# Kernel tuning notes

Hardware: AMD Instinct MI355X
Metric: run time of the kernel (lower is better)

## Reference

```python
import jax, jax.numpy as jnp
import numpy as np

WS = 7          # window size
SHIFT = 3       # shift size (window_size // 2)
RES = 56        # input resolution
DIMS = 192      # channel dim
HEADS = DIMS // 32
HD = DIMS // HEADS
N = WS * WS     # tokens per window (49)
NW = (RES // WS) ** 2  # windows per image (64)


def _position_index():
    # matches tf.meshgrid(coords_w, coords_h)[::-1] stacking
    coords = np.stack(np.meshgrid(np.arange(WS), np.arange(WS))[::-1])  # (2, ws, ws)
    flat = coords.reshape(2, -1)                                        # (2, N)
    rel = (flat[:, :, None] - flat[:, None, :]).transpose(1, 2, 0)      # (N, N, 2)
    h = (rel[..., 0] + WS - 1) * (2 * WS - 1)
    w = rel[..., 1] + WS - 1
    return (h + w).reshape(-1)                                          # (N*N,)


def _swin_mask():
    img = np.zeros((RES, RES))
    cnt = 0
    sls = (slice(0, -WS), slice(-WS, -SHIFT), slice(-SHIFT, None))
    for hs in sls:
        for ws_ in sls:
            img[hs, ws_] = cnt
            cnt += 1
    # window partition
    m = img.reshape(RES // WS, WS, RES // WS, WS).transpose(0, 2, 1, 3).reshape(-1, N)
    a = m[:, None, :] - m[:, :, None]            # (nW, N, N)
    a = np.where(a == 0, 0.0, -1000.0).astype(np.float32)
    return a[:, None]                            # (nW, 1, N, N)


_PIDX = _position_index()
_MASK = _swin_mask()


def setup_inputs() -> dict:
    key = jax.random.key(0)
    ks = jax.random.split(key, 6)
    s = 0.02
    return {
        "x": jax.random.normal(ks[0], (64, RES, RES, DIMS), jnp.float32),
        "table": jax.random.normal(ks[1], ((2 * WS - 1) ** 2, HEADS), jnp.float32) * s,
        "wq": jax.random.normal(ks[2], (DIMS, DIMS), jnp.float32) * s,
        "bq": jnp.zeros((DIMS,), jnp.float32),
        "wk": jax.random.normal(ks[3], (DIMS, DIMS), jnp.float32) * s,
        "bk": jnp.zeros((DIMS,), jnp.float32),
        "wv": jax.random.normal(ks[4], (DIMS, DIMS), jnp.float32) * s,
        "bv": jnp.zeros((DIMS,), jnp.float32),
        "wo": jax.random.normal(ks[5], (DIMS, DIMS), jnp.float32) * s,
        "bo": jnp.zeros((DIMS,), jnp.float32),
    }


def reference(x, table, wq, bq, wk, bk, wv, bv, wo, bo):
    B = x.shape[0]
    # gathered relative-position bias: (1, heads, N, N)
    bias = table[_PIDX].reshape(N, N, HEADS).transpose(2, 0, 1)[None]
    mask = jnp.asarray(_MASK)  # (nW, 1, N, N)

    # cyclic shift + window partition
    xs = jnp.roll(x, (-SHIFT, -SHIFT), axis=(1, 2))
    xw = xs.reshape(B, RES // WS, WS, RES // WS, WS, DIMS)
    xw = xw.transpose(0, 1, 3, 2, 4, 5).reshape(-1, N, DIMS)  # (B*nW, N, C)
    BW = xw.shape[0]

    def split_heads(t):
        return t.reshape(BW, N, HEADS, HD).transpose(0, 2, 1, 3)  # (BW, h, N, hd)

    q = split_heads(xw @ wq + bq)
    k = split_heads(xw @ wk + bk)
    v = split_heads(xw @ wv + bv)

    scores = jnp.einsum('bhqd,bhkd->bhqk', q, k) / jnp.sqrt(jnp.float32(HD))
    scores = scores + bias
    # matches tf.repeat(mask, B // W, axis=0) in the original code
    scores = scores + jnp.repeat(mask, BW // NW, axis=0)
    attn = jax.nn.softmax(scores, axis=-1)
    o = jnp.einsum('bhqk,bhkd->bhqd', attn, v)
    o = o.transpose(0, 2, 1, 3).reshape(BW, N, DIMS)
    o = o @ wo + bo

    # window reverse + reverse cyclic shift
    o = o.reshape(B, RES // WS, RES // WS, WS, WS, DIMS)
    o = o.transpose(0, 1, 3, 2, 4, 5).reshape(B, RES, RES, DIMS)
    return jnp.roll(o, (SHIFT, SHIFT), axis=(1, 2))
```

## Files before the change

### kernel.cpp

```cpp
#include <hip/hip_runtime.h>


typedef __attribute__((ext_vector_type(8))) short bf16x8;
typedef __attribute__((ext_vector_type(4))) short short4v;
typedef __attribute__((ext_vector_type(4))) float f32x4;

__device__ __forceinline__ short f2bf(float x) {
  unsigned u = __builtin_bit_cast(unsigned, x);
  u += 0x7fffu + ((u >> 16) & 1u);
  return (short)(u >> 16);
}

__global__ void prep_kernel(const float* __restrict__ wq, const float* __restrict__ wk,
                            const float* __restrict__ wv, const float* __restrict__ wo,
                            const float* __restrict__ table,
                            short* __restrict__ wT, float* __restrict__ biasx) {
  int tid = blockIdx.x * 256 + threadIdx.x;
  if (tid < 4 * 36864) {
    int mat = tid / 36864, rem = tid % 36864;
    int k = rem / 192, n = rem % 192;
    const float* w = (mat == 0) ? wq : (mat == 1) ? wk : (mat == 2) ? wv : wo;
    wT[mat * 36864 + n * 192 + k] = f2bf(w[k * 192 + n]);
  }
  if (tid < 6 * 2401) {
    int h = tid / 2401, rem = tid % 2401;
    int q = rem / 49, k = rem % 49;
    int idx = ((q / 7) - (k / 7) + 6) * 13 + ((q % 7) - (k % 7) + 6);
    biasx[tid] = table[idx * 6 + h];
  }
}

__launch_bounds__(768, 3)
__global__ void swin_attn_kernel(const float* __restrict__ x,
                                 const short* __restrict__ wT,
                                 const float* __restrict__ biasx,
                                 const float* __restrict__ bq, const float* __restrict__ bk,
                                 const float* __restrict__ bv, const float* __restrict__ bo,
                                 float* __restrict__ out) {
  extern __shared__ short smem[];
  short* s_xw = smem;
  short* s_q  = smem + 12800;
  short* s_k  = smem + 25600;
  short* s_vt = smem + 38400;
  short* s_p  = smem + 52224;

  const int tid  = threadIdx.x;
  const int w    = tid >> 6;
  const int lane = tid & 63;
  const int quad = lane >> 4;
  const int l15  = lane & 15;

  const int bw  = blockIdx.x;
  const int b   = bw >> 6;
  const int wi  = bw & 63;
  const int wwh = wi >> 3, www = wi & 7;
  const int mwh = b >> 3,  mww = b & 7;

  for (int i = tid; i < 49 * 48; i += 768) {
    int t = i / 48, c4 = i - t * 48;
    int th = t / 7, tw = t - th * 7;
    int gh = wwh * 7 + th + 3; if (gh >= 56) gh -= 56;
    int gw = www * 7 + tw + 3; if (gw >= 56) gw -= 56;
    const float4 v = *(const float4*)(x + (((b * 56 + gh) * 56 + gw) * 192 + c4 * 4));
    short4v s;
    ((short*)&s)[0] = f2bf(v.x); ((short*)&s)[1] = f2bf(v.y);
    ((short*)&s)[2] = f2bf(v.z); ((short*)&s)[3] = f2bf(v.w);
    *(short4v*)(s_xw + t * 200 + c4 * 4) = s;
  }
  __syncthreads();

  const f32x4 zero4 = {0.f, 0.f, 0.f, 0.f};

  {
    const int mat = w >> 2;
    const short* wt = wT + mat * 36864;
    const float* bias = (mat == 0) ? bq : (mat == 1) ? bk : bv;

    bf16x8 axw[4][6];
#pragma unroll
    for (int mt = 0; mt < 4; ++mt)
#pragma unroll
      for (int ks = 0; ks < 6; ++ks)
        axw[mt][ks] = *(const bf16x8*)(s_xw + (mt * 16 + l15) * 200 + ks * 32 + quad * 8);

#pragma unroll
    for (int i = 0; i < 3; ++i) {
      const int col = ((w & 3) * 3 + i) * 16 + l15;
      f32x4 acc[4] = {zero4, zero4, zero4, zero4};
#pragma unroll
      for (int ks = 0; ks < 6; ++ks) {
        bf16x8 bfr = *(const bf16x8*)(wt + col * 192 + ks * 32 + quad * 8);
#pragma unroll
        for (int mt = 0; mt < 4; ++mt)
          acc[mt] = __builtin_amdgcn_mfma_f32_16x16x32_bf16(axw[mt][ks], bfr, acc[mt], 0, 0, 0);
      }
      const float bv_ = bias[col];
      if (mat < 2) {
        short* dst = (mat == 0) ? s_q : s_k;
#pragma unroll
        for (int mt = 0; mt < 4; ++mt)
#pragma unroll
          for (int r = 0; r < 4; ++r)
            dst[(mt * 16 + quad * 4 + r) * 200 + col] = f2bf(acc[mt][r] + bv_);
      } else {
#pragma unroll
        for (int mt = 0; mt < 4; ++mt) {
          short4v vv;
#pragma unroll
          for (int r = 0; r < 4; ++r) {
            int m = mt * 16 + quad * 4 + r;
            float val = (m < 49) ? (acc[mt][r] + bv_) : 0.f;
            ((short*)&vv)[r] = f2bf(val);
          }
          *(short4v*)(s_vt + col * 72 + mt * 16 + quad * 4) = vv;
        }
      }
    }
  }
  __syncthreads();

  const int rt = w & 3;
  const int hp = w >> 2;

  int cm[4], mclamp[4];
#pragma unroll
  for (int r = 0; r < 4; ++r) {
    int m = rt * 16 + quad * 4 + r;
    int mm = (m < 49) ? m : 48;
    mclamp[r] = mm * 49;
    int th = mm / 7, tw = mm - th * 7;
    int ch = (mwh == 7) ? (1 + (th >= 4)) : 0;
    int cw = (mww == 7) ? (1 + (tw >= 4)) : 0;
    cm[r] = ch * 3 + cw;
  }
  int cn[4], nclamp[4], nvalid[4];
#pragma unroll
  for (int nt = 0; nt < 4; ++nt) {
    int n = nt * 16 + l15;
    nvalid[nt] = (n < 49);
    int nn = nvalid[nt] ? n : 48;
    nclamp[nt] = nn;
    int th = nn / 7, tw = nn - th * 7;
    int ch = (mwh == 7) ? (1 + (th >= 4)) : 0;
    int cw = (mww == 7) ? (1 + (tw >= 4)) : 0;
    cn[nt] = ch * 3 + cw;
  }

  short* my_p = s_p + w * (16 * 72);
  const float SCALE = 0.17677669529663687f;
  const float NEGINF = -__builtin_inff();

#pragma unroll
  for (int hh = 0; hh < 2; ++hh) {
    const int h = hp * 2 + hh;
    const int d0 = h * 32;
    bf16x8 qf = *(const bf16x8*)(s_q + (rt * 16 + l15) * 200 + d0 + quad * 8);
    float sv[4][4];
#pragma unroll
    for (int nt = 0; nt < 4; ++nt) {
      bf16x8 kf = *(const bf16x8*)(s_k + (nt * 16 + l15) * 200 + d0 + quad * 8);
      f32x4 sfr = __builtin_amdgcn_mfma_f32_16x16x32_bf16(qf, kf, zero4, 0, 0, 0);
#pragma unroll
      for (int r = 0; r < 4; ++r) {
        float v = sfr[r] * SCALE + biasx[h * 2401 + mclamp[r] + nclamp[nt]]
                + ((cm[r] == cn[nt]) ? 0.f : -1000.f);
        sv[nt][r] = nvalid[nt] ? v : NEGINF;
      }
    }
    float inv[4];
#pragma unroll
    for (int r = 0; r < 4; ++r) {
      float mx = fmaxf(fmaxf(sv[0][r], sv[1][r]), fmaxf(sv[2][r], sv[3][r]));
#pragma unroll
      for (int d = 1; d < 16; d <<= 1) mx = fmaxf(mx, __shfl_xor(mx, d));
      float s0 = 0.f;
#pragma unroll
      for (int nt = 0; nt < 4; ++nt) {
        float e = __expf(sv[nt][r] - mx);
        sv[nt][r] = e;
        s0 += e;
      }
#pragma unroll
      for (int d = 1; d < 16; d <<= 1) s0 += __shfl_xor(s0, d);
      inv[r] = 1.0f / s0;
    }
#pragma unroll
    for (int nt = 0; nt < 4; ++nt)
#pragma unroll
      for (int r = 0; r < 4; ++r)
        my_p[(quad * 4 + r) * 72 + nt * 16 + l15] = f2bf(sv[nt][r]);

    f32x4 of[2] = {zero4, zero4};
#pragma unroll
    for (int ks = 0; ks < 2; ++ks) {
      bf16x8 pf = *(const bf16x8*)(my_p + l15 * 72 + ks * 32 + quad * 8);
#pragma unroll
      for (int nt2 = 0; nt2 < 2; ++nt2) {
        bf16x8 vf = *(const bf16x8*)(s_vt + (d0 + nt2 * 16 + l15) * 72 + ks * 32 + quad * 8);
        of[nt2] = __builtin_amdgcn_mfma_f32_16x16x32_bf16(pf, vf, of[nt2], 0, 0, 0);
      }
    }
#pragma unroll
    for (int nt2 = 0; nt2 < 2; ++nt2)
#pragma unroll
      for (int r = 0; r < 4; ++r)
        s_xw[(rt * 16 + quad * 4 + r) * 200 + d0 + nt2 * 16 + l15] = f2bf(of[nt2][r] * inv[r]);
  }
  __syncthreads();

  const int cg = hp;

  bf16x8 ao[6];
#pragma unroll
  for (int ks = 0; ks < 6; ++ks)
    ao[ks] = *(const bf16x8*)(s_xw + (rt * 16 + l15) * 200 + ks * 32 + quad * 8);

  int rowbase[4], rvalid[4];
#pragma unroll
  for (int r = 0; r < 4; ++r) {
    int m = rt * 16 + quad * 4 + r;
    rvalid[r] = (m < 49);
    int mm = rvalid[r] ? m : 0;
    int th = mm / 7, tw = mm - th * 7;
    int gh = wwh * 7 + th + 3; if (gh >= 56) gh -= 56;
    int gw = www * 7 + tw + 3; if (gw >= 56) gw -= 56;
    rowbase[r] = ((b * 56 + gh) * 56 + gw) * 192;
  }

  const short* wto = wT + 3 * 36864;
#pragma unroll
  for (int i = 0; i < 4; ++i) {
    const int col = (cg * 4 + i) * 16 + l15;
    f32x4 acc = zero4;
#pragma unroll
    for (int ks = 0; ks < 6; ++ks) {
      bf16x8 bfr = *(const bf16x8*)(wto + col * 192 + ks * 32 + quad * 8);
      acc = __builtin_amdgcn_mfma_f32_16x16x32_bf16(ao[ks], bfr, acc, 0, 0, 0);
    }
    const float bo_ = bo[col];
#pragma unroll
    for (int r = 0; r < 4; ++r)
      if (rvalid[r]) out[rowbase[r] + col] = acc[r] + bo_;
  }
}

extern "C" void kernel_launch(void* const* d_in, const int* in_sizes, int n_in,
                              void* d_out, int out_size, void* d_ws, size_t ws_size,
                              hipStream_t stream) {
  const float* x     = (const float*)d_in[0];
  const float* table = (const float*)d_in[1];
  const float* wq    = (const float*)d_in[2];
  const float* bq    = (const float*)d_in[3];
  const float* wk    = (const float*)d_in[4];
  const float* bk    = (const float*)d_in[5];
  const float* wv    = (const float*)d_in[6];
  const float* bv    = (const float*)d_in[7];
  const float* wo    = (const float*)d_in[8];
  const float* bo    = (const float*)d_in[9];
  float* out = (float*)d_out;

  short* wT    = (short*)d_ws;
  float* biasx = (float*)((char*)d_ws + 294912);

  prep_kernel<<<576, 256, 0, stream>>>(wq, wk, wv, wo, table, wT, biasx);

  const int smem_bytes = 66048 * 2;
  (void)hipFuncSetAttribute(reinterpret_cast<const void*>(swin_attn_kernel),
                            hipFuncAttributeMaxDynamicSharedMemorySize, smem_bytes);
  swin_attn_kernel<<<4096, 768, smem_bytes, stream>>>(x, wT, biasx, bq, bk, bv, bo, out);
}
```

Before: 589.0 us.

## Make attention kernel persistent over 16 windows with double-buffered input prefetch

Each block now processes 16 windows of one image in a loop instead of one window, launching 256 blocks instead of 4096. The next window's input is loaded into registers during attention and written to the alternate shared buffer, overlapping global loads with compute. Bias and mask terms are precomputed once per block in registers, and the QKV and output projections are remapped so each wave owns a token row tile with transposed MFMA operands, giving vectorized stores. The cost is only 256 blocks on a large GPU, roughly one block per CU, plus higher register pressure from the cached bias and prefetch registers.

```diff
diff --git a/kernel.cpp b/kernel.cpp
--- a/kernel.cpp
+++ b/kernel.cpp
@@ -38,11 +38,11 @@
                                  const float* __restrict__ bv, const float* __restrict__ bo,
                                  float* __restrict__ out) {
   extern __shared__ short smem[];
-  short* s_xw = smem;
-  short* s_q  = smem + 12800;
-  short* s_k  = smem + 25600;
-  short* s_vt = smem + 38400;
-  short* s_p  = smem + 52224;
+  short* bufA = smem;
+  short* bufB = smem + 13824;
+  short* s_q  = smem + 27648;
+  short* s_k  = smem + 40448;
+  short* s_vt = smem + 53248;
 
   const int tid  = threadIdx.x;
   const int w    = tid >> 6;
@@ -50,197 +50,269 @@
   const int quad = lane >> 4;
   const int l15  = lane & 15;
 
-  const int bw  = blockIdx.x;
-  const int b   = bw >> 6;
-  const int wi  = bw & 63;
-  const int wwh = wi >> 3, www = wi & 7;
-  const int mwh = b >> 3,  mww = b & 7;
-
-  for (int i = tid; i < 49 * 48; i += 768) {
+  const int p   = blockIdx.x;
+  const int b   = p >> 2;
+  const int mwh = b >> 3, mww = b & 7;
+
+  const int rt = w & 3;
+  const int g  = w >> 2;
+
+  const f32x4 zero4 = {0.f, 0.f, 0.f, 0.f};
+  const float NEGINF = -__builtin_inff();
+  const float SCALE = 0.17677669529663687f;
+
+  int th_[4], tw_[4], wa_[4], c4_[4];
+#pragma unroll
+  for (int it = 0; it < 4; ++it) {
+    int i = tid + it * 768;
     int t = i / 48, c4 = i - t * 48;
-    int th = t / 7, tw = t - th * 7;
-    int gh = wwh * 7 + th + 3; if (gh >= 56) gh -= 56;
-    int gw = www * 7 + tw + 3; if (gw >= 56) gw -= 56;
-    const float4 v = *(const float4*)(x + (((b * 56 + gh) * 56 + gw) * 192 + c4 * 4));
-    short4v s;
-    ((short*)&s)[0] = f2bf(v.x); ((short*)&s)[1] = f2bf(v.y);
-    ((short*)&s)[2] = f2bf(v.z); ((short*)&s)[3] = f2bf(v.w);
-    *(short4v*)(s_xw + t * 200 + c4 * 4) = s;
+    th_[it] = t / 7; tw_[it] = t - th_[it] * 7;
+    c4_[it] = c4; wa_[it] = t * 200 + c4 * 4;
+  }
+  const bool has4 = (tid < 48);
+
+  const int token = rt * 16 + l15;
+  const bool tokv = (token < 49);
+
+  const int qc  = tokv ? token : 48;
+  const int qth = qc / 7, qtw = qc - qth * 7;
+  const int cq  = ((mwh == 7) ? (1 + (qth >= 4)) : 0) * 3
+                + ((mww == 7) ? (1 + (qtw >= 4)) : 0);
+  float bm[2][4][4];
+#pragma unroll
+  for (int hh = 0; hh < 2; ++hh) {
+    const int h = g * 2 + hh;
+#pragma unroll
+    for (int mt = 0; mt < 4; ++mt)
+#pragma unroll
+      for (int r = 0; r < 4; ++r) {
+        int key = mt * 16 + quad * 4 + r;
+        if (key > 48) {
+          bm[hh][mt][r] = NEGINF;
+        } else {
+          int kth = key / 7, ktw = key - kth * 7;
+          int ck = ((mwh == 7) ? (1 + (kth >= 4)) : 0) * 3
+                 + ((mww == 7) ? (1 + (ktw >= 4)) : 0);
+          bm[hh][mt][r] = biasx[h * 2401 + qc * 49 + key] + ((ck == cq) ? 0.f : -1000.f);
+        }
+      }
+  }
+
+  const int tt  = tokv ? token : 0;
+  const int tth = tt / 7, ttw = tt - tth * 7;
+
+  {
+    const int wi0 = (p & 3) * 16;
+    const int hb = (wi0 >> 3) * 7 + 3, wb = (wi0 & 7) * 7 + 3;
+#pragma unroll
+    for (int it = 0; it < 3; ++it) {
+      int gh = hb + th_[it]; if (gh >= 56) gh -= 56;
+      int gw = wb + tw_[it]; if (gw >= 56) gw -= 56;
+      float4 v = *(const float4*)(x + (((b * 56 + gh) * 56 + gw) * 192 + c4_[it] * 4));
+      short4v s;
+      s[0] = f2bf(v.x); s[1] = f2bf(v.y); s[2] = f2bf(v.z); s[3] = f2bf(v.w);
+      *(short4v*)(bufA + wa_[it]) = s;
+    }
+    if (has4) {
+      int gh = hb + th_[3]; if (gh >= 56) gh -= 56;
+      int gw = wb + tw_[3]; if (gw >= 56) gw -= 56;
+      float4 v = *(const float4*)(x + (((b * 56 + gh) * 56 + gw) * 192 + c4_[3] * 4));
+      short4v s;
+      s[0] = f2bf(v.x); s[1] = f2bf(v.y); s[2] = f2bf(v.z); s[3] = f2bf(v.w);
+      *(short4v*)(bufA + wa_[3]) = s;
+    }
   }
   __syncthreads();
 
-  const f32x4 zero4 = {0.f, 0.f, 0.f, 0.f};
-
-  {
-    const int mat = w >> 2;
-    const short* wt = wT + mat * 36864;
-    const float* bias = (mat == 0) ? bq : (mat == 1) ? bk : bv;
-
-    bf16x8 axw[4][6];
-#pragma unroll
-    for (int mt = 0; mt < 4; ++mt)
-#pragma unroll
-      for (int ks = 0; ks < 6; ++ks)
-        axw[mt][ks] = *(const bf16x8*)(s_xw + (mt * 16 + l15) * 200 + ks * 32 + quad * 8);
-
-#pragma unroll
-    for (int i = 0; i < 3; ++i) {
-      const int col = ((w & 3) * 3 + i) * 16 + l15;
-      f32x4 acc[4] = {zero4, zero4, zero4, zero4};
+  float4 px0, px1, px2, px3;
+
+#pragma unroll 1
+  for (int win = 0; win < 16; ++win) {
+    short* xw   = (win & 1) ? bufB : bufA;
+    short* pbuf = (win & 1) ? bufA : bufB;
+    const int wi  = (p & 3) * 16 + win;
+    const int wwh = wi >> 3, www = wi & 7;
+
+    bf16x8 xf[6];
+#pragma unroll
+    for (int ks = 0; ks < 6; ++ks)
+      xf[ks] = *(const bf16x8*)(xw + (rt * 16 + l15) * 200 + ks * 32 + quad * 8);
+
+#pragma unroll
+    for (int mat = 0; mat < 2; ++mat) {
+      const short* wt = wT + mat * 36864;
+      const float* bp = mat ? bk : bq;
+      short* dst = mat ? s_k : s_q;
+#pragma unroll
+      for (int j = 0; j < 4; ++j) {
+        const int dbase = (g * 4 + j) * 16;
+        const short* wrow = wt + (dbase + l15) * 192;
+        f32x4 acc = zero4;
+#pragma unroll
+        for (int ks = 0; ks < 6; ++ks) {
+          bf16x8 wfr = *(const bf16x8*)(wrow + ks * 32 + quad * 8);
+          acc = __builtin_amdgcn_mfma_f32_16x16x32_bf16(wfr, xf[ks], acc, 0, 0, 0);
+        }
+        const float4 b4 = *(const float4*)(bp + dbase + quad * 4);
+        short4v st;
+        st[0] = f2bf(tokv ? acc[0] + b4.x : 0.f);
+        st[1] = f2bf(tokv ? acc[1] + b4.y : 0.f);
+        st[2] = f2bf(tokv ? acc[2] + b4.z : 0.f);
+        st[3] = f2bf(tokv ? acc[3] + b4.w : 0.f);
+        *(short4v*)(dst + (rt * 16 + l15) * 200 + dbase + quad * 4) = st;
+      }
+    }
+    {
+      const short* wt = wT + 2 * 36864;
+#pragma unroll
+      for (int j = 0; j < 4; ++j) {
+        const int dbase = (g * 4 + j) * 16;
+        const short* wrow = wt + (dbase + l15) * 192;
+        f32x4 acc = zero4;
+#pragma unroll
+        for (int ks = 0; ks < 6; ++ks) {
+          bf16x8 wfr = *(const bf16x8*)(wrow + ks * 32 + quad * 8);
+          acc = __builtin_amdgcn_mfma_f32_16x16x32_bf16(xf[ks], wfr, acc, 0, 0, 0);
+        }
+        const float bvv = bv[dbase + l15];
+        short4v st;
+#pragma unroll
+        for (int r = 0; r < 4; ++r) {
+          int key = rt * 16 + quad * 4 + r;
+          st[r] = f2bf((key < 49) ? (acc[r] + bvv) : 0.f);
+        }
+        *(short4v*)(s_vt + (dbase + l15) * 72 + rt * 16 + quad * 4) = st;
+      }
+    }
+    __syncthreads();
+
+    if (win < 15) {
+      const int wi2 = wi + 1;
+      const int hb = (wi2 >> 3) * 7 + 3, wb = (wi2 & 7) * 7 + 3;
+      {
+        int gh = hb + th_[0]; if (gh >= 56) gh -= 56;
+        int gw = wb + tw_[0]; if (gw >= 56) gw -= 56;
+        px0 = *(const float4*)(x + (((b * 56 + gh) * 56 + gw) * 192 + c4_[0] * 4));
+      }
+      {
+        int gh = hb + th_[1]; if (gh >= 56) gh -= 56;
+        int gw = wb + tw_[1]; if (gw >= 56) gw -= 56;
+        px1 = *(const float4*)(x + (((b * 56 + gh) * 56 + gw) * 192 + c4_[1] * 4));
+      }
+      {
+        int gh = hb + th_[2]; if (gh >= 56) gh -= 56;
+        int gw = wb + tw_[2]; if (gw >= 56) gw -= 56;
+        px2 = *(const float4*)(x + (((b * 56 + gh) * 56 + gw) * 192 + c4_[2] * 4));
+      }
+      if (has4) {
+        int gh = hb + th_[3]; if (gh >= 56) gh -= 56;
+        int gw = wb + tw_[3]; if (gw >= 56) gw -= 56;
+        px3 = *(const float4*)(x + (((b * 56 + gh) * 56 + gw) * 192 + c4_[3] * 4));
+      }
+    }
+
+    short* myp = pbuf + w * 1152;
+#pragma unroll
+    for (int hh = 0; hh < 2; ++hh) {
+      const int d0 = (g * 2 + hh) * 32;
+      bf16x8 qf = *(const bf16x8*)(s_q + (rt * 16 + l15) * 200 + d0 + quad * 8);
+      float sv[4][4];
+#pragma unroll
+      for (int mt = 0; mt < 4; ++mt) {
+        bf16x8 kf = *(const bf16x8*)(s_k + (mt * 16 + l15) * 200 + d0 + quad * 8);
+        f32x4 s = __builtin_amdgcn_mfma_f32_16x16x32_bf16(kf, qf, zero4, 0, 0, 0);
+#pragma unroll
+        for (int r = 0; r < 4; ++r)
+          sv[mt][r] = s[r] * SCALE + bm[hh][mt][r];
+      }
+      float mx = sv[0][0];
+#pragma unroll
+      for (int mt = 0; mt < 4; ++mt)
+#pragma unroll
+        for (int r = 0; r < 4; ++r) mx = fmaxf(mx, sv[mt][r]);
+      mx = fmaxf(mx, __shfl_xor(mx, 16));
+      mx = fmaxf(mx, __shfl_xor(mx, 32));
+      float s0 = 0.f;
+#pragma unroll
+      for (int mt = 0; mt < 4; ++mt)
+#pragma unroll
+        for (int r = 0; r < 4; ++r) {
+          float e = __expf(sv[mt][r] - mx);
+          sv[mt][r] = e;
+          s0 += e;
+        }
+      s0 += __shfl_xor(s0, 16);
+      s0 += __shfl_xor(s0, 32);
+      const float inv = 1.0f / s0;
+#pragma unroll
+      for (int mt = 0; mt < 4; ++mt) {
+        short4v st;
+#pragma unroll
+        for (int r = 0; r < 4; ++r) st[r] = f2bf(sv[mt][r]);
+        *(short4v*)(myp + l15 * 72 + mt * 16 + quad * 4) = st;
+      }
+#pragma unroll
+      for (int mt2 = 0; mt2 < 2; ++mt2) {
+        f32x4 o = zero4;
+#pragma unroll
+        for (int ks = 0; ks < 2; ++ks) {
+          bf16x8 vfr = *(const bf16x8*)(s_vt + (d0 + mt2 * 16 + l15) * 72 + ks * 32 + quad * 8);
+          bf16x8 pfr = *(const bf16x8*)(myp + l15 * 72 + ks * 32 + quad * 8);
+          o = __builtin_amdgcn_mfma_f32_16x16x32_bf16(vfr, pfr, o, 0, 0, 0);
+        }
+        short4v st;
+#pragma unroll
+        for (int r = 0; r < 4; ++r) st[r] = f2bf(o[r] * inv);
+        *(short4v*)(xw + (rt * 16 + l15) * 200 + d0 + mt2 * 16 + quad * 4) = st;
+      }
+    }
+    __syncthreads();
+
+    bf16x8 ao[6];
+#pragma unroll
+    for (int ks = 0; ks < 6; ++ks)
+      ao[ks] = *(const bf16x8*)(xw + (rt * 16 + l15) * 200 + ks * 32 + quad * 8);
+
+    if (win < 15) {
+      short4v s;
+      s[0] = f2bf(px0.x); s[1] = f2bf(px0.y); s[2] = f2bf(px0.z); s[3] = f2bf(px0.w);
+      *(short4v*)(pbuf + wa_[0]) = s;
+      s[0] = f2bf(px1.x); s[1] = f2bf(px1.y); s[2] = f2bf(px1.z); s[3] = f2bf(px1.w);
+      *(short4v*)(pbuf + wa_[1]) = s;
+      s[0] = f2bf(px2.x); s[1] = f2bf(px2.y); s[2] = f2bf(px2.z); s[3] = f2bf(px2.w);
+      *(short4v*)(pbuf + wa_[2]) = s;
+      if (has4) {
+        s[0] = f2bf(px3.x); s[1] = f2bf(px3.y); s[2] = f2bf(px3.z); s[3] = f2bf(px3.w);
+        *(short4v*)(pbuf + wa_[3]) = s;
+      }
+    }
+
+    int rowbase = 0;
+    if (tokv) {
+      int gh = wwh * 7 + tth + 3; if (gh >= 56) gh -= 56;
+      int gw = www * 7 + ttw + 3; if (gw >= 56) gw -= 56;
+      rowbase = ((b * 56 + gh) * 56 + gw) * 192;
+    }
+    const short* wto = wT + 3 * 36864;
+#pragma unroll
+    for (int j = 0; j < 4; ++j) {
+      const int cbase = (g * 4 + j) * 16;
+      const short* wrow = wto + (cbase + l15) * 192;
+      f32x4 acc = zero4;
 #pragma unroll
       for (int ks = 0; ks < 6; ++ks) {
-        bf16x8 bfr = *(const bf16x8*)(wt + col * 192 + ks * 32 + quad * 8);
-#pragma unroll
-        for (int mt = 0; mt < 4; ++mt)
-          acc[mt] = __builtin_amdgcn_mfma_f32_16x16x32_bf16(axw[mt][ks], bfr, acc[mt], 0, 0, 0);
-      }
-      const float bv_ = bias[col];
-      if (mat < 2) {
-        short* dst = (mat == 0) ? s_q : s_k;
-#pragma unroll
-        for (int mt = 0; mt < 4; ++mt)
-#pragma unroll
-          for (int r = 0; r < 4; ++r)
-            dst[(mt * 16 + quad * 4 + r) * 200 + col] = f2bf(acc[mt][r] + bv_);
-      } else {
-#pragma unroll
-        for (int mt = 0; mt < 4; ++mt) {
-          short4v vv;
-#pragma unroll
-          for (int r = 0; r < 4; ++r) {
-            int m = mt * 16 + quad * 4 + r;
-            float val = (m < 49) ? (acc[mt][r] + bv_) : 0.f;
-            ((short*)&vv)[r] = f2bf(val);
-          }
-          *(short4v*)(s_vt + col * 72 + mt * 16 + quad * 4) = vv;
-        }
-      }
-    }
-  }
-  __syncthreads();
-
-  const int rt = w & 3;
-  const int hp = w >> 2;
-
-  int cm[4], mclamp[4];
-#pragma unroll
-  for (int r = 0; r < 4; ++r) {
-    int m = rt * 16 + quad * 4 + r;
-    int mm = (m < 49) ? m : 48;
-    mclamp[r] = mm * 49;
-    int th = mm / 7, tw = mm - th * 7;
-    int ch = (mwh == 7) ? (1 + (th >= 4)) : 0;
-    int cw = (mww == 7) ? (1 + (tw >= 4)) : 0;
-    cm[r] = ch * 3 + cw;
-  }
-  int cn[4], nclamp[4], nvalid[4];
-#pragma unroll
-  for (int nt = 0; nt < 4; ++nt) {
-    int n = nt * 16 + l15;
-    nvalid[nt] = (n < 49);
-    int nn = nvalid[nt] ? n : 48;
-    nclamp[nt] = nn;
-    int th = nn / 7, tw = nn - th * 7;
-    int ch = (mwh == 7) ? (1 + (th >= 4)) : 0;
-    int cw = (mww == 7) ? (1 + (tw >= 4)) : 0;
-    cn[nt] = ch * 3 + cw;
-  }
-
-  short* my_p = s_p + w * (16 * 72);
-  const float SCALE = 0.17677669529663687f;
-  const float NEGINF = -__builtin_inff();
-
-#pragma unroll
-  for (int hh = 0; hh < 2; ++hh) {
-    const int h = hp * 2 + hh;
-    const int d0 = h * 32;
-    bf16x8 qf = *(const bf16x8*)(s_q + (rt * 16 + l15) * 200 + d0 + quad * 8);
-    float sv[4][4];
-#pragma unroll
-    for (int nt = 0; nt < 4; ++nt) {
-      bf16x8 kf = *(const bf16x8*)(s_k + (nt * 16 + l15) * 200 + d0 + quad * 8);
-      f32x4 sfr = __builtin_amdgcn_mfma_f32_16x16x32_bf16(qf, kf, zero4, 0, 0, 0);
-#pragma unroll
-      for (int r = 0; r < 4; ++r) {
-        float v = sfr[r] * SCALE + biasx[h * 2401 + mclamp[r] + nclamp[nt]]
-                + ((cm[r] == cn[nt]) ? 0.f : -1000.f);
-        sv[nt][r] = nvalid[nt] ? v : NEGINF;
-      }
-    }
-    float inv[4];
-#pragma unroll
-    for (int r = 0; r < 4; ++r) {
-      float mx = fmaxf(fmaxf(sv[0][r], sv[1][r]), fmaxf(sv[2][r], sv[3][r]));
-#pragma unroll
-      for (int d = 1; d < 16; d <<= 1) mx = fmaxf(mx, __shfl_xor(mx, d));
-      float s0 = 0.f;
-#pragma unroll
-      for (int nt = 0; nt < 4; ++nt) {
-        float e = __expf(sv[nt][r] - mx);
-        sv[nt][r] = e;
-        s0 += e;
-      }
-#pragma unroll
-      for (int d = 1; d < 16; d <<= 1) s0 += __shfl_xor(s0, d);
-      inv[r] = 1.0f / s0;
-    }
-#pragma unroll
-    for (int nt = 0; nt < 4; ++nt)
-#pragma unroll
-      for (int r = 0; r < 4; ++r)
-        my_p[(quad * 4 + r) * 72 + nt * 16 + l15] = f2bf(sv[nt][r]);
-
-    f32x4 of[2] = {zero4, zero4};
-#pragma unroll
-    for (int ks = 0; ks < 2; ++ks) {
-      bf16x8 pf = *(const bf16x8*)(my_p + l15 * 72 + ks * 32 + quad * 8);
-#pragma unroll
-      for (int nt2 = 0; nt2 < 2; ++nt2) {
-        bf16x8 vf = *(const bf16x8*)(s_vt + (d0 + nt2 * 16 + l15) * 72 + ks * 32 + quad * 8);
-        of[nt2] = __builtin_amdgcn_mfma_f32_16x16x32_bf16(pf, vf, of[nt2], 0, 0, 0);
-      }
-    }
-#pragma unroll
-    for (int nt2 = 0; nt2 < 2; ++nt2)
-#pragma unroll
-      for (int r = 0; r < 4; ++r)
-        s_xw[(rt * 16 + quad * 4 + r) * 200 + d0 + nt2 * 16 + l15] = f2bf(of[nt2][r] * inv[r]);
-  }
-  __syncthreads();
-
-  const int cg = hp;
-
-  bf16x8 ao[6];
-#pragma unroll
-  for (int ks = 0; ks < 6; ++ks)
-    ao[ks] = *(const bf16x8*)(s_xw + (rt * 16 + l15) * 200 + ks * 32 + quad * 8);
-
-  int rowbase[4], rvalid[4];
-#pragma unroll
-  for (int r = 0; r < 4; ++r) {
-    int m = rt * 16 + quad * 4 + r;
-    rvalid[r] = (m < 49);
-    int mm = rvalid[r] ? m : 0;
-    int th = mm / 7, tw = mm - th * 7;
-    int gh = wwh * 7 + th + 3; if (gh >= 56) gh -= 56;
-    int gw = www * 7 + tw + 3; if (gw >= 56) gw -= 56;
-    rowbase[r] = ((b * 56 + gh) * 56 + gw) * 192;
-  }
-
-  const short* wto = wT + 3 * 36864;
-#pragma unroll
-  for (int i = 0; i < 4; ++i) {
-    const int col = (cg * 4 + i) * 16 + l15;
-    f32x4 acc = zero4;
-#pragma unroll
-    for (int ks = 0; ks < 6; ++ks) {
-      bf16x8 bfr = *(const bf16x8*)(wto + col * 192 + ks * 32 + quad * 8);
-      acc = __builtin_amdgcn_mfma_f32_16x16x32_bf16(ao[ks], bfr, acc, 0, 0, 0);
-    }
-    const float bo_ = bo[col];
-#pragma unroll
-    for (int r = 0; r < 4; ++r)
-      if (rvalid[r]) out[rowbase[r] + col] = acc[r] + bo_;
+        bf16x8 wfr = *(const bf16x8*)(wrow + ks * 32 + quad * 8);
+        acc = __builtin_amdgcn_mfma_f32_16x16x32_bf16(wfr, ao[ks], acc, 0, 0, 0);
+      }
+      const float4 b4 = *(const float4*)(bo + cbase + quad * 4);
+      if (tokv) {
+        float4 v;
+        v.x = acc[0] + b4.x; v.y = acc[1] + b4.y;
+        v.z = acc[2] + b4.z; v.w = acc[3] + b4.w;
+        *(float4*)(out + rowbase + cbase + quad * 4) = v;
+      }
+    }
+    __syncthreads();
   }
 }
 
@@ -264,8 +336,8 @@
 
   prep_kernel<<<576, 256, 0, stream>>>(wq, wk, wv, wo, table, wT, biasx);
 
-  const int smem_bytes = 66048 * 2;
+  const int smem_bytes = 67072 * 2;
   (void)hipFuncSetAttribute(reinterpret_cast<const void*>(swin_attn_kernel),
                             hipFuncAttributeMaxDynamicSharedMemorySize, smem_bytes);
-  swin_attn_kernel<<<4096, 768, smem_bytes, stream>>>(x, wT, biasx, bq, bk, bv, bo, out);
+  swin_attn_kernel<<<256, 768, smem_bytes, stream>>>(x, wT, biasx, bq, bk, bv, bo, out);
 }
```

Result: slower. 1.386 ms (+135.4%).
